# Kernel tuning notes

Measured on AMD Instinct MI355X. Metric: run time of the kernel, lower is better.

Reference implementation:

```python
import jax, jax.numpy as jnp
import numpy as np

# ----- config (mirrors SpatialAxis init) -----
B, N = 1, 32768
D_MODEL, NHEAD, DEPTH = 256, 8, 2
COORD = 3
PATCH = 512          # self.patch_size default
BITS = 10            # self.morton_bits default
SHIFT = True         # self.shift_order default
MLP_H = 4 * D_MODEL
HD = D_MODEL // NHEAD
EPS = 1e-5


def _part1by2(v):
    # spread low 10 bits of int32 so there are 2 zero bits between each
    v = v & 0x000003FF
    v = (v | (v << 16)) & 0x030000FF
    v = (v | (v << 8)) & 0x0300F00F
    v = (v | (v << 4)) & 0x030C30C3
    v = (v | (v << 2)) & 0x09249249
    return v


def _perm_for_block(coords, i):
    # Z-order (Morton) serialization with per-block axis rotation; odd blocks
    # shift the order by half a patch (shifted-window style). Returns [B,N] int32.
    c = jax.lax.stop_gradient(coords)[..., np.roll(np.arange(COORD), -i)]
    cmin = c.min(axis=1, keepdims=True)
    cmax = c.max(axis=1, keepdims=True)
    q = ((c - cmin) / (cmax - cmin + 1e-9) * (2 ** BITS - 1)).astype(jnp.int32)
    q = jnp.clip(q, 0, 2 ** BITS - 1)
    code = (_part1by2(q[..., 0]) | (_part1by2(q[..., 1]) << 1)
            | (_part1by2(q[..., 2]) << 2))  # [B,N]
    perm = jnp.argsort(code, axis=1)
    if SHIFT and (i % 2 == 1):
        perm = jnp.roll(perm, PATCH // 2, axis=1)
    return perm


def _ln(x, g, b):
    m = x.mean(-1, keepdims=True)
    v = x.var(-1, keepdims=True)
    return (x - m) * jax.lax.rsqrt(v + EPS) * g + b


def _point_block(xs, cs, p):
    # xs: [M, P, D] tokens of one patch each; cs: [M, P, 3]
    M, P, D = xs.shape
    h = _ln(xs, p['ln1_g'], p['ln1_b'])
    qkv = h @ p['w_qkv'] + p['b_qkv']                         # [M,P,3D]
    q, k, v = jnp.split(qkv, 3, axis=-1)
    q = q.reshape(M, P, NHEAD, HD)
    k = k.reshape(M, P, NHEAD, HD)
    v = v.reshape(M, P, NHEAD, HD)
    scores = jnp.einsum('mphd,mqhd->mhpq', q, k) / np.sqrt(HD).astype(np.float32)
    rel = cs[:, :, None, :] - cs[:, None, :, :]               # [M,P,P,3]
    bias = jnp.einsum('mpqc,ch->mhpq', rel, p['w_pos']) + p['b_pos'][None, :, None, None]
    attn = jax.nn.softmax(scores + bias, axis=-1)
    o = jnp.einsum('mhpq,mqhd->mphd', attn, v).reshape(M, P, D)
    xs = xs + o @ p['w_proj'] + p['b_proj']
    h2 = _ln(xs, p['ln2_g'], p['ln2_b'])
    xs = xs + jax.nn.gelu(h2 @ p['w_fc1'] + p['b_fc1']) @ p['w_fc2'] + p['b_fc2']
    return xs


def _forward(x, coords, params):
    Cc = coords.shape[-1]
    nblk = N // PATCH
    for i in range(DEPTH):
        p = {k: v[i] for k, v in params.items()}
        perm = _perm_for_block(coords, i)                      # [B,N]
        inv = jnp.argsort(perm, axis=1)
        x_s = jnp.take_along_axis(x, perm[:, :, None], axis=1)
        c_s = jnp.take_along_axis(coords, perm[:, :, None], axis=1)
        x_f = x_s.reshape(B * nblk, PATCH, D_MODEL)
        c_f = c_s.reshape(B * nblk, PATCH, Cc)
        y = _point_block(x_f, c_f, p).reshape(B, N, D_MODEL)
        x = jnp.take_along_axis(y, inv[:, :, None], axis=1)
    return _ln(x, params['norm_g'][0], params['norm_b'][0])


def setup_inputs() -> dict:
    key = jax.random.key(0)
    ks = jax.random.split(key, 20)
    s = 0.02
    d = {
        'x': jax.random.normal(ks[0], (B, N, D_MODEL), jnp.float32),
        'coords': jax.random.uniform(ks[1], (B, N, COORD), jnp.float32),
        'ln1_g': jnp.ones((DEPTH, D_MODEL), jnp.float32),
        'ln1_b': jnp.zeros((DEPTH, D_MODEL), jnp.float32),
        'w_qkv': jax.random.normal(ks[2], (DEPTH, D_MODEL, 3 * D_MODEL), jnp.float32) * s,
        'b_qkv': jnp.zeros((DEPTH, 3 * D_MODEL), jnp.float32),
        'w_proj': jax.random.normal(ks[3], (DEPTH, D_MODEL, D_MODEL), jnp.float32) * s,
        'b_proj': jnp.zeros((DEPTH, D_MODEL), jnp.float32),
        'w_pos': jax.random.normal(ks[4], (DEPTH, COORD, NHEAD), jnp.float32) * s,
        'b_pos': jnp.zeros((DEPTH, NHEAD), jnp.float32),
        'ln2_g': jnp.ones((DEPTH, D_MODEL), jnp.float32),
        'ln2_b': jnp.zeros((DEPTH, D_MODEL), jnp.float32),
        'w_fc1': jax.random.normal(ks[5], (DEPTH, D_MODEL, MLP_H), jnp.float32) * s,
        'b_fc1': jnp.zeros((DEPTH, MLP_H), jnp.float32),
        'w_fc2': jax.random.normal(ks[6], (DEPTH, MLP_H, D_MODEL), jnp.float32) * s,
        'b_fc2': jnp.zeros((DEPTH, D_MODEL), jnp.float32),
        'norm_g': jnp.ones((1, D_MODEL), jnp.float32),
        'norm_b': jnp.zeros((1, D_MODEL), jnp.float32),
    }
    return d


def reference(x, coords, ln1_g, ln1_b, w_qkv, b_qkv, w_proj, b_proj, w_pos, b_pos,
              ln2_g, ln2_b, w_fc1, b_fc1, w_fc2, b_fc2, norm_g, norm_b):
    params = dict(ln1_g=ln1_g, ln1_b=ln1_b, w_qkv=w_qkv, b_qkv=b_qkv,
                  w_proj=w_proj, b_proj=b_proj, w_pos=w_pos, b_pos=b_pos,
                  ln2_g=ln2_g, ln2_b=ln2_b, w_fc1=w_fc1, b_fc1=b_fc1,
                  w_fc2=w_fc2, b_fc2=b_fc2, norm_g=norm_g, norm_b=norm_b)
    return _forward(x, coords, params)
```

## Files before the change

kernel.cpp:

```cpp
#include <hip/hip_runtime.h>

typedef unsigned long long u64;
typedef unsigned int u32;
typedef unsigned short u16;
typedef float f32x4 __attribute__((ext_vector_type(4)));
typedef __bf16 bf16x8 __attribute__((ext_vector_type(8)));

#define N_TOK 32768

__device__ inline u16 f2bf(float f){
  u32 x = __float_as_uint(f);
  u32 r = x + 0x7FFFu + ((x >> 16) & 1u);
  return (u16)(r >> 16);
}

__device__ inline f32x4 mfma16(bf16x8 a, bf16x8 b, f32x4 c){
  return __builtin_amdgcn_mfma_f32_16x16x32_bf16(a, b, c, 0, 0, 0);
}

typedef const __attribute__((address_space(1))) unsigned int* gas_ptr;
typedef __attribute__((address_space(3))) unsigned int* las_ptr;
__device__ inline void gload_lds16(const u16* g, u16* l){
  __builtin_amdgcn_global_load_lds((gas_ptr)g, (las_ptr)l, 16, 0, 0);
}

__device__ inline u32 rp_idx(const u64* __restrict__ keys, int j, int shift){
  return (u32)(keys[(j + N_TOK - shift) & (N_TOK - 1)] & 0xFFFFull);
}

__device__ inline float gelu_tanh(float x){
  float u = 0.7978845608028654f * (x + 0.044715f * x * x * x);
  float e = __expf(2.0f * u);
  return 0.5f * x * (2.0f - 2.0f / (e + 1.0f));
}

__device__ inline u32 part1by2(u32 v){
  v &= 0x3FFu;
  v = (v | (v << 16)) & 0x030000FFu;
  v = (v | (v << 8))  & 0x0300F00Fu;
  v = (v | (v << 4))  & 0x030C30C3u;
  v = (v | (v << 2))  & 0x09249249u;
  return v;
}

__device__ inline void ce64(u64& a, u64& b, bool asc){
  u64 lo = a < b ? a : b;
  u64 hi = a < b ? b : a;
  a = asc ? lo : hi;
  b = asc ? hi : lo;
}

__global__ void __launch_bounds__(1024) minmax_kernel(const float* __restrict__ coords,
                                                      float* __restrict__ cmm){
  float mn[3] = {1e30f,1e30f,1e30f}, mx[3] = {-1e30f,-1e30f,-1e30f};
  for (int t = threadIdx.x; t < N_TOK; t += 1024){
    #pragma unroll
    for (int a = 0; a < 3; ++a){
      float v = coords[t*3 + a];
      mn[a] = fminf(mn[a], v); mx[a] = fmaxf(mx[a], v);
    }
  }
  #pragma unroll
  for (int a = 0; a < 3; ++a){
    for (int m = 1; m < 64; m <<= 1){
      mn[a] = fminf(mn[a], __shfl_xor(mn[a], m));
      mx[a] = fmaxf(mx[a], __shfl_xor(mx[a], m));
    }
  }
  __shared__ float smn[16][3], smx[16][3];
  int w = threadIdx.x >> 6, lane = threadIdx.x & 63;
  if (lane == 0){
    #pragma unroll
    for (int a = 0; a < 3; ++a){ smn[w][a] = mn[a]; smx[w][a] = mx[a]; }
  }
  __syncthreads();
  if (threadIdx.x == 0){
    for (int i = 1; i < 16; ++i)
      for (int a = 0; a < 3; ++a){
        smn[0][a] = fminf(smn[0][a], smn[i][a]);
        smx[0][a] = fmaxf(smx[0][a], smx[i][a]);
      }
    for (int a = 0; a < 3; ++a){ cmm[a] = smn[0][a]; cmm[3+a] = smx[0][a]; }
  }
}

__global__ void __launch_bounds__(256) wprep_kernel(const float* __restrict__ src,
                                                    u16* __restrict__ dst, int K, int Nn){
  int layer = blockIdx.y;
  src += (size_t)layer * K * Nn;
  dst += (size_t)layer * K * Nn;
  int ntx = Nn >> 5;
  int tk = blockIdx.x / ntx, tn = blockIdx.x % ntx;
  __shared__ float tile[32][33];
  int r = threadIdx.x >> 5, c = threadIdx.x & 31;
  for (int rr = r; rr < 32; rr += 8)
    tile[rr][c] = src[(size_t)(tk*32 + rr) * Nn + tn*32 + c];
  __syncthreads();
  for (int rr = r; rr < 32; rr += 8)
    dst[(size_t)(tn*32 + rr) * K + tk*32 + c] = f2bf(tile[c][rr]);
}

__global__ void __launch_bounds__(256) codes_kernel(const float* __restrict__ coords,
                                                    const float* __restrict__ cmm,
                                                    u64* __restrict__ keys){
  int p = blockIdx.x * 256 + threadIdx.x;
  int layer = p >> 15, t = p & (N_TOK - 1);
  u32 code = 0;
  #pragma unroll
  for (int j = 0; j < 3; ++j){
    int ax = (j + layer) % 3;
    float c = coords[t*3 + ax];
    float mn = cmm[ax], mx = cmm[3 + ax];
    float v = (c - mn) / (mx - mn + 1e-9f) * 1023.0f;
    int q = (int)v;
    q = q < 0 ? 0 : (q > 1023 ? 1023 : q);
    code |= part1by2((u32)q) << j;
  }
  keys[p] = ((u64)code << 16) | (u32)t;
}

__global__ void __launch_bounds__(512) bitonic_local_sort8k(u64* __restrict__ keys){
  __shared__ u64 s[8192];
  int base = blockIdx.x * 8192;
  int tid = threadIdx.x;
  {
    int c = tid * 16;
    u64 v[16];
    #pragma unroll
    for (int p = 0; p < 16; ++p) v[p] = keys[base + c + p];
    #pragma unroll
    for (int k2 = 2; k2 <= 16; k2 <<= 1){
      #pragma unroll
      for (int j = k2 >> 1; j > 0; j >>= 1){
        #pragma unroll
        for (int p = 0; p < 16; ++p){
          if ((p & j) == 0){
            bool asc = ((((base + c + p) & (N_TOK-1)) & k2) == 0);
            ce64(v[p], v[p+j], asc);
          }
        }
      }
    }
    #pragma unroll
    for (int p = 0; p < 16; ++p) s[c + p] = v[p];
  }
  __syncthreads();
  for (int k = 32; k <= 8192; k <<= 1){
    int j = k >> 1;
    while (j >= 16){
      if (j >= 32){
        int j2 = j >> 1;
        int bb[4]; bool aa[4]; u64 e[4][4];
        #pragma unroll
        for (int it = 0; it < 4; ++it){
          int g = tid + it*512;
          int lo = g & (j2 - 1);
          int b = ((g ^ lo) << 2) | lo;
          bb[it] = b;
          aa[it] = ((((base + b) & (N_TOK-1)) & k) == 0);
          e[it][0] = s[b]; e[it][1] = s[b + j2]; e[it][2] = s[b + j]; e[it][3] = s[b + j + j2];
        }
        #pragma unroll
        for (int it = 0; it < 4; ++it){
          ce64(e[it][0], e[it][2], aa[it]); ce64(e[it][1], e[it][3], aa[it]);
          ce64(e[it][0], e[it][1], aa[it]); ce64(e[it][2], e[it][3], aa[it]);
          s[bb[it]] = e[it][0]; s[bb[it]+j2] = e[it][1];
          s[bb[it]+j] = e[it][2]; s[bb[it]+j+j2] = e[it][3];
        }
        j >>= 2;
      } else {
        int ii[8]; bool aa[8]; u64 ea[8], eb[8];
        #pragma unroll
        for (int it = 0; it < 8; ++it){
          int pr = tid + it*512;
          int i = ((pr & ~15) << 1) | (pr & 15);
          ii[it] = i;
          aa[it] = ((((base + i) & (N_TOK-1)) & k) == 0);
          ea[it] = s[i]; eb[it] = s[i + 16];
        }
        #pragma unroll
        for (int it = 0; it < 8; ++it){
          ce64(ea[it], eb[it], aa[it]);
          s[ii[it]] = ea[it]; s[ii[it]+16] = eb[it];
        }
        j >>= 1;
      }
      __syncthreads();
    }
    {
      int c = tid * 16;
      bool asc = ((((base + c) & (N_TOK-1)) & k) == 0);
      u64 v[16];
      #pragma unroll
      for (int p = 0; p < 16; ++p) v[p] = s[c + p];
      #pragma unroll
      for (int j2 = 8; j2 > 0; j2 >>= 1){
        #pragma unroll
        for (int p = 0; p < 16; ++p)
          if ((p & j2) == 0) ce64(v[p], v[p+j2], asc);
      }
      if (k == 8192){
        #pragma unroll
        for (int p = 0; p < 16; ++p) keys[base + c + p] = v[p];
      } else {
        #pragma unroll
        for (int p = 0; p < 16; ++p) s[c + p] = v[p];
        __syncthreads();
      }
    }
  }
}

__global__ void __launch_bounds__(256) bitonic_global_step(u64* __restrict__ keys, int j, int k){
  int p = blockIdx.x * 256 + threadIdx.x;
  int layer = p >> 14, pl = p & 16383;
  int i = ((pl & ~(j-1)) << 1) | (pl & (j-1));
  int l = i + j;
  bool asc = ((i & k & (N_TOK-1)) == 0);
  u64* kp = keys + (layer << 15);
  u64 a = kp[i], b = kp[l];
  if ((a > b) == asc){ kp[i] = b; kp[l] = a; }
}

__global__ void __launch_bounds__(512) bitonic_local_merge8k(u64* __restrict__ keys, int k){
  __shared__ u64 s[8192];
  int base = blockIdx.x * 8192;
  int tid = threadIdx.x;
  for (int i = tid; i < 8192; i += 512) s[i] = keys[base + i];
  __syncthreads();
  int j = 4096;
  while (j >= 16){
    if (j >= 32){
      int j2 = j >> 1;
      int bb[4]; bool aa[4]; u64 e[4][4];
      #pragma unroll
      for (int it = 0; it < 4; ++it){
        int g = tid + it*512;
        int lo = g & (j2 - 1);
        int b = ((g ^ lo) << 2) | lo;
        bb[it] = b;
        aa[it] = ((((base + b) & (N_TOK-1)) & k) == 0);
        e[it][0] = s[b]; e[it][1] = s[b + j2]; e[it][2] = s[b + j]; e[it][3] = s[b + j + j2];
      }
      #pragma unroll
      for (int it = 0; it < 4; ++it){
        ce64(e[it][0], e[it][2], aa[it]); ce64(e[it][1], e[it][3], aa[it]);
        ce64(e[it][0], e[it][1], aa[it]); ce64(e[it][2], e[it][3], aa[it]);
        s[bb[it]] = e[it][0]; s[bb[it]+j2] = e[it][1];
        s[bb[it]+j] = e[it][2]; s[bb[it]+j+j2] = e[it][3];
      }
      j >>= 2;
    } else {
      int ii[8]; bool aa[8]; u64 ea[8], eb[8];
      #pragma unroll
      for (int it = 0; it < 8; ++it){
        int pr = tid + it*512;
        int i = ((pr & ~15) << 1) | (pr & 15);
        ii[it] = i;
        aa[it] = ((((base + i) & (N_TOK-1)) & k) == 0);
        ea[it] = s[i]; eb[it] = s[i + 16];
      }
      #pragma unroll
      for (int it = 0; it < 8; ++it){
        ce64(ea[it], eb[it], aa[it]);
        s[ii[it]] = ea[it]; s[ii[it]+16] = eb[it];
      }
      j >>= 1;
    }
    __syncthreads();
  }
  int c = tid * 16;
  bool asc = ((((base + c) & (N_TOK-1)) & k) == 0);
  u64 v[16];
  #pragma unroll
  for (int p = 0; p < 16; ++p) v[p] = s[c + p];
  #pragma unroll
  for (int j2 = 8; j2 > 0; j2 >>= 1){
    #pragma unroll
    for (int p = 0; p < 16; ++p)
      if ((p & j2) == 0) ce64(v[p], v[p+j2], asc);
  }
  #pragma unroll
  for (int p = 0; p < 16; ++p) keys[base + c + p] = v[p];
}

__global__ void __launch_bounds__(256) gather_ln1_kernel(
    const float* __restrict__ xin, const float* __restrict__ coords,
    const u64* __restrict__ keys, int shift,
    const float* __restrict__ g1, const float* __restrict__ b1,
    const float* __restrict__ wpos,
    float* __restrict__ dproj, u16* __restrict__ h){
  int w = threadIdx.x >> 6, lane = threadIdx.x & 63;
  int j = blockIdx.x * 4 + w;
  u32 src = rp_idx(keys, j, shift);
  float4 v = ((const float4*)xin)[(size_t)src * 64 + lane];
  float s = v.x + v.y + v.z + v.w;
  for (int m = 1; m < 64; m <<= 1) s += __shfl_xor(s, m);
  float mean = s * (1.0f / 256.0f);
  float dx = v.x - mean, dy = v.y - mean, dz = v.z - mean, dw = v.w - mean;
  float q = dx*dx + dy*dy + dz*dz + dw*dw;
  for (int m = 1; m < 64; m <<= 1) q += __shfl_xor(q, m);
  float rs = rsqrtf(q * (1.0f / 256.0f) + 1e-5f);
  int c0 = lane * 4;
  u16 h0 = f2bf(dx * rs * g1[c0+0] + b1[c0+0]);
  u16 h1 = f2bf(dy * rs * g1[c0+1] + b1[c0+1]);
  u16 h2 = f2bf(dz * rs * g1[c0+2] + b1[c0+2]);
  u16 h3 = f2bf(dw * rs * g1[c0+3] + b1[c0+3]);
  uint2 pk; pk.x = (u32)h0 | ((u32)h1 << 16); pk.y = (u32)h2 | ((u32)h3 << 16);
  *(uint2*)&h[(size_t)j * 256 + c0] = pk;
  if (lane < 8){
    float acc = 0.0f;
    #pragma unroll
    for (int c = 0; c < 3; ++c) acc += coords[(size_t)src*3 + c] * wpos[c*8 + lane];
    dproj[(size_t)j * 8 + lane] = acc;
  }
}

__global__ void __launch_bounds__(256) ln_bf16_kernel(const float* __restrict__ xin,
    const float* __restrict__ g, const float* __restrict__ b, u16* __restrict__ out){
  int w = threadIdx.x >> 6, lane = threadIdx.x & 63;
  int j = blockIdx.x * 4 + w;
  float4 v = ((const float4*)xin)[(size_t)j * 64 + lane];
  float s = v.x + v.y + v.z + v.w;
  for (int m = 1; m < 64; m <<= 1) s += __shfl_xor(s, m);
  float mean = s * (1.0f / 256.0f);
  float dx = v.x - mean, dy = v.y - mean, dz = v.z - mean, dw = v.w - mean;
  float q = dx*dx + dy*dy + dz*dz + dw*dw;
  for (int m = 1; m < 64; m <<= 1) q += __shfl_xor(q, m);
  float rs = rsqrtf(q * (1.0f / 256.0f) + 1e-5f);
  int c0 = lane * 4;
  u16 h0 = f2bf(dx * rs * g[c0+0] + b[c0+0]);
  u16 h1 = f2bf(dy * rs * g[c0+1] + b[c0+1]);
  u16 h2 = f2bf(dz * rs * g[c0+2] + b[c0+2]);
  u16 h3 = f2bf(dw * rs * g[c0+3] + b[c0+3]);
  uint2 pk; pk.x = (u32)h0 | ((u32)h1 << 16); pk.y = (u32)h2 | ((u32)h3 << 16);
  *(uint2*)&out[(size_t)j * 256 + c0] = pk;
}

__global__ void __launch_bounds__(256) ln_final_kernel(const float* __restrict__ xin,
    const float* __restrict__ g, const float* __restrict__ b, float* __restrict__ out){
  int w = threadIdx.x >> 6, lane = threadIdx.x & 63;
  int j = blockIdx.x * 4 + w;
  float4 v = ((const float4*)xin)[(size_t)j * 64 + lane];
  float s = v.x + v.y + v.z + v.w;
  for (int m = 1; m < 64; m <<= 1) s += __shfl_xor(s, m);
  float mean = s * (1.0f / 256.0f);
  float dx = v.x - mean, dy = v.y - mean, dz = v.z - mean, dw = v.w - mean;
  float q = dx*dx + dy*dy + dz*dz + dw*dw;
  for (int m = 1; m < 64; m <<= 1) q += __shfl_xor(q, m);
  float rs = rsqrtf(q * (1.0f / 256.0f) + 1e-5f);
  int c0 = lane * 4;
  float4 o;
  o.x = dx * rs * g[c0+0] + b[c0+0];
  o.y = dy * rs * g[c0+1] + b[c0+1];
  o.z = dz * rs * g[c0+2] + b[c0+2];
  o.w = dw * rs * g[c0+3] + b[c0+3];
  ((float4*)out)[(size_t)j * 64 + lane] = o;
}

template<int EPI>
__global__ void __launch_bounds__(256) gemm_kernel(
    const u16* __restrict__ A, const u16* __restrict__ Wt,
    const float* __restrict__ bias, int K, int Nn,
    u16* __restrict__ outb, float* __restrict__ outf,
    const float* __restrict__ res, const u64* __restrict__ keys, int shift){
  __shared__ __align__(16) u16 As[2][128 * 32];
  __shared__ __align__(16) u16 Bs[2][128 * 32];
  int m0 = blockIdx.x * 128;
  int n0 = blockIdx.y * 128;
  int tid = threadIdx.x;
  int lane = tid & 63, lc = lane & 15, g = lane >> 4;
  int w = tid >> 6, wm = w >> 1, wn = w & 1;
  f32x4 acc[4][4];
  #pragma unroll
  for (int mi = 0; mi < 4; ++mi)
    #pragma unroll
    for (int ni = 0; ni < 4; ++ni) acc[mi][ni] = (f32x4){0.f,0.f,0.f,0.f};
  int r1 = tid >> 2, s1 = tid & 3;
  int r2 = r1 + 64;
  const u16* Ag1 = A  + (size_t)(m0 + r1) * K + s1*8;
  const u16* Ag2 = A  + (size_t)(m0 + r2) * K + s1*8;
  const u16* Bg1 = Wt + (size_t)(n0 + r1) * K + s1*8;
  const u16* Bg2 = Wt + (size_t)(n0 + r2) * K + s1*8;
  int wofs = (tid & ~63) * 8;
  int nt = K >> 5;
  gload_lds16(Ag1, As[0] + wofs);
  gload_lds16(Ag2, As[0] + wofs + 2048);
  gload_lds16(Bg1, Bs[0] + wofs);
  gload_lds16(Bg2, Bs[0] + wofs + 2048);
  __syncthreads();
  int cur = 0;
  for (int t = 0; t < nt; ++t){
    if (t + 1 < nt){
      int kk = (t + 1) << 5;
      gload_lds16(Ag1 + kk, As[cur^1] + wofs);
      gload_lds16(Ag2 + kk, As[cur^1] + wofs + 2048);
      gload_lds16(Bg1 + kk, Bs[cur^1] + wofs);
      gload_lds16(Bg2 + kk, Bs[cur^1] + wofs + 2048);
    }
    bf16x8 af[4], bfr[4];
    #pragma unroll
    for (int mi = 0; mi < 4; ++mi)
      af[mi] = *(const bf16x8*)&As[cur][(wm*64 + mi*16 + lc)*32 + g*8];
    #pragma unroll
    for (int ni = 0; ni < 4; ++ni)
      bfr[ni] = *(const bf16x8*)&Bs[cur][(wn*64 + ni*16 + lc)*32 + g*8];
    #pragma unroll
    for (int mi = 0; mi < 4; ++mi)
      #pragma unroll
      for (int ni = 0; ni < 4; ++ni)
        acc[mi][ni] = mfma16(af[mi], bfr[ni], acc[mi][ni]);
    __syncthreads();
    cur ^= 1;
  }
  #pragma unroll
  for (int ni = 0; ni < 4; ++ni){
    int col = n0 + wn*64 + ni*16 + lc;
    float bv = bias[col];
    #pragma unroll
    for (int mi = 0; mi < 4; ++mi){
      #pragma unroll
      for (int r = 0; r < 4; ++r){
        int row = m0 + wm*64 + mi*16 + g*4 + r;
        float v = acc[mi][ni][r] + bv;
        if constexpr (EPI == 0){
          if (col < 256) v *= 0.25500526f;
          outb[(size_t)row * Nn + col] = f2bf(v);
        } else if constexpr (EPI == 1){
          outb[(size_t)row * Nn + col] = f2bf(gelu_tanh(v));
        } else if constexpr (EPI == 2){
          u32 src = rp_idx(keys, row, shift);
          outf[(size_t)row * 256 + col] = res[(size_t)src * 256 + col] + v;
        } else {
          u32 dst = rp_idx(keys, row, shift);
          outf[(size_t)dst * 256 + col] = res[(size_t)row * 256 + col] + v;
        }
      }
    }
  }
}

#define VSTR 516
#define ATTN_LDS (512*40*2 + 32*VSTR*2 + 512*2)
__global__ void __launch_bounds__(512) attn_kernel(
    const u16* __restrict__ qkvb, const float* __restrict__ dproj,
    u16* __restrict__ o){
  extern __shared__ char smem[];
  u16* Kl = (u16*)smem;
  u16* Vt = (u16*)(smem + 512*40*2);
  u16* wl = (u16*)(smem + 512*40*2 + 32*VSTR*2);
  int h = blockIdx.x & 7;
  int base = (blockIdx.x >> 3) * 512;
  int tid = threadIdx.x, w = tid >> 6, lane = tid & 63, lc = lane & 15, g = lane >> 4;
  const float L2E = 1.4426950408889634f;
  for (int i = tid; i < 2048; i += 512){
    int j = i >> 2, s = i & 3;
    *(uint4*)&Kl[j*40 + s*8] =
      *(const uint4*)&qkvb[(size_t)(base + j)*768 + 256 + h*32 + s*8];
  }
  for (int i = tid; i < 1024; i += 512){
    int p = i >> 2, d0 = (i & 3) * 8;
    int j0 = 2*p, j1 = j0 + 1;
    float wv0 = exp2f(-L2E * dproj[(size_t)(base + j0)*8 + h]);
    float wv1 = exp2f(-L2E * dproj[(size_t)(base + j1)*8 + h]);
    uint4 r0 = *(const uint4*)&qkvb[(size_t)(base + j0)*768 + 512 + h*32 + d0];
    uint4 r1 = *(const uint4*)&qkvb[(size_t)(base + j1)*768 + 512 + h*32 + d0];
    const u16* p0 = (const u16*)&r0; const u16* p1 = (const u16*)&r1;
    int j5 = j0 & 31, b = j5 >> 4, m = j5 & 15;
    int slot = (j0 & ~31) + 8*(m >> 2) + 4*b + (m & 3);
    #pragma unroll
    for (int e = 0; e < 8; ++e){
      float f0 = __uint_as_float(((u32)p0[e]) << 16) * wv0;
      float f1 = __uint_as_float(((u32)p1[e]) << 16) * wv1;
      u32 pk;
      asm("v_cvt_pk_bf16_f32 %0, %1, %2" : "=v"(pk) : "v"(f0), "v"(f1));
      *(u32*)&Vt[(d0 + e)*VSTR + slot] = pk;
    }
    if (d0 == 0){
      u32 pkw;
      asm("v_cvt_pk_bf16_f32 %0, %1, %2" : "=v"(pkw) : "v"(wv0), "v"(wv1));
      *(u32*)&wl[slot] = pkw;
    }
  }
  __syncthreads();
  const f32x4 zf = {0.f,0.f,0.f,0.f};
  const bf16x8 zb = {};
  const u16* Qg = qkvb + (size_t)base*768 + h*32;
  for (int t = 0; t < 4; ++t){
    int q0 = w*64 + t*16;
    bf16x8 qf = *(const bf16x8*)&Qg[(size_t)(q0 + lc)*768 + g*8];
    f32x4 o0 = zf, o1 = zf, lacc = zf;
    #pragma unroll 4
    for (int grp = 0; grp < 16; ++grp){
      int kb = grp * 32;
      bf16x8 kf0 = *(const bf16x8*)&Kl[(kb + lc)*40 + g*8];
      bf16x8 kf1 = *(const bf16x8*)&Kl[(kb + 16 + lc)*40 + g*8];
      f32x4 s0 = mfma16(kf0, qf, zf);
      f32x4 s1 = mfma16(kf1, qf, zf);
      #pragma unroll
      for (int r = 0; r < 4; ++r){
        s0[r] = exp2f(s0[r]);
        s1[r] = exp2f(s1[r]);
      }
      u32 pk0, pk1, pk2, pk3;
      asm("v_cvt_pk_bf16_f32 %0, %1, %2" : "=v"(pk0) : "v"(s0[0]), "v"(s0[1]));
      asm("v_cvt_pk_bf16_f32 %0, %1, %2" : "=v"(pk1) : "v"(s0[2]), "v"(s0[3]));
      asm("v_cvt_pk_bf16_f32 %0, %1, %2" : "=v"(pk2) : "v"(s1[0]), "v"(s1[1]));
      asm("v_cvt_pk_bf16_f32 %0, %1, %2" : "=v"(pk3) : "v"(s1[2]), "v"(s1[3]));
      bf16x8 pf;
      ((u32*)&pf)[0] = pk0; ((u32*)&pf)[1] = pk1;
      ((u32*)&pf)[2] = pk2; ((u32*)&pf)[3] = pk3;
      bf16x8 v0, v1;
      *(uint2*)&v0       = *(const uint2*)&Vt[lc*VSTR + kb + g*8];
      *((uint2*)&v0 + 1) = *(const uint2*)&Vt[lc*VSTR + kb + g*8 + 4];
      *(uint2*)&v1       = *(const uint2*)&Vt[(16+lc)*VSTR + kb + g*8];
      *((uint2*)&v1 + 1) = *(const uint2*)&Vt[(16+lc)*VSTR + kb + g*8 + 4];
      bf16x8 wf = *(const bf16x8*)&wl[kb + g*8];
      bf16x8 wfz = (lc == 0) ? wf : zb;
      __builtin_amdgcn_s_setprio(1);
      o0 = mfma16(pf, v0, o0);
      o1 = mfma16(pf, v1, o1);
      lacc = mfma16(pf, wfz, lacc);
      __builtin_amdgcn_s_setprio(0);
    }
    #pragma unroll
    for (int r = 0; r < 4; ++r){
      float l = __shfl(lacc[r], lane & 48);
      float inv = 1.0f / l;
      size_t tok = (size_t)(base + q0 + g*4 + r);
      o[tok*256 + h*32 + lc]      = f2bf(o0[r] * inv);
      o[tok*256 + h*32 + 16 + lc] = f2bf(o1[r] * inv);
    }
  }
}

extern "C" void kernel_launch(void* const* d_in, const int* in_sizes, int n_in,
                              void* d_out, int out_size, void* d_ws, size_t ws_size,
                              hipStream_t stream){
  const float* x      = (const float*)d_in[0];
  const float* coords = (const float*)d_in[1];
  const float* ln1_g  = (const float*)d_in[2];
  const float* ln1_b  = (const float*)d_in[3];
  const float* w_qkv  = (const float*)d_in[4];
  const float* b_qkv  = (const float*)d_in[5];
  const float* w_proj = (const float*)d_in[6];
  const float* b_proj = (const float*)d_in[7];
  const float* w_pos  = (const float*)d_in[8];
  const float* ln2_g  = (const float*)d_in[10];
  const float* ln2_b  = (const float*)d_in[11];
  const float* w_fc1  = (const float*)d_in[12];
  const float* b_fc1  = (const float*)d_in[13];
  const float* w_fc2  = (const float*)d_in[14];
  const float* b_fc2  = (const float*)d_in[15];
  const float* norm_g = (const float*)d_in[16];
  const float* norm_b = (const float*)d_in[17];
  float* outp = (float*)d_out;

  hipFuncSetAttribute((const void*)attn_kernel,
                      hipFuncAttributeMaxDynamicSharedMemorySize, ATTN_LDS);

  char* ws = (char*)d_ws;
  size_t off = 0;
  auto alloc = [&](size_t bytes) -> void* {
    void* p = ws + off;
    off += (bytes + 255) & ~(size_t)255;
    return p;
  };
  u64*   keys   = (u64*)  alloc((size_t)2 * N_TOK * 8);
  float* cmm    = (float*)alloc(256);
  float* dproj  = (float*)alloc((size_t)N_TOK * 8 * 4);
  u16*   h      = (u16*)  alloc((size_t)N_TOK * 256 * 2);
  u16*   qkvb   = (u16*)  alloc((size_t)N_TOK * 768 * 2);
  float* x2     = (float*)alloc((size_t)N_TOK * 256 * 4);
  u16*   t      = (u16*)  alloc((size_t)N_TOK * 1024 * 2);
  float* xA     = (float*)alloc((size_t)N_TOK * 256 * 4);
  u16*   wtqkv  = (u16*)  alloc((size_t)2 * 256 * 768 * 2);
  u16*   wtproj = (u16*)  alloc((size_t)2 * 256 * 256 * 2);
  u16*   wtfc1  = (u16*)  alloc((size_t)2 * 256 * 1024 * 2);
  u16*   wtfc2  = (u16*)  alloc((size_t)2 * 1024 * 256 * 2);
  u16*   o      = t;
  float* xB     = (float*)qkvb;
  (void)in_sizes; (void)n_in; (void)out_size; (void)ws_size;

  minmax_kernel<<<1, 1024, 0, stream>>>(coords, cmm);
  wprep_kernel<<<dim3(8*24, 2),  256, 0, stream>>>(w_qkv,  wtqkv,  256, 768);
  wprep_kernel<<<dim3(8*8, 2),   256, 0, stream>>>(w_proj, wtproj, 256, 256);
  wprep_kernel<<<dim3(8*32, 2),  256, 0, stream>>>(w_fc1,  wtfc1,  256, 1024);
  wprep_kernel<<<dim3(32*8, 2),  256, 0, stream>>>(w_fc2,  wtfc2,  1024, 256);

  codes_kernel<<<256, 256, 0, stream>>>(coords, cmm, keys);
  bitonic_local_sort8k<<<8, 512, 0, stream>>>(keys);
  bitonic_global_step<<<128, 256, 0, stream>>>(keys, 8192, 16384);
  bitonic_local_merge8k<<<8, 512, 0, stream>>>(keys, 16384);
  bitonic_global_step<<<128, 256, 0, stream>>>(keys, 16384, 32768);
  bitonic_global_step<<<128, 256, 0, stream>>>(keys, 8192, 32768);
  bitonic_local_merge8k<<<8, 512, 0, stream>>>(keys, 32768);

  for (int layer = 0; layer < 2; ++layer){
    int shift = (layer & 1) ? 256 : 0;
    const float* xin = (layer == 0) ? x : xA;
    float* xout = (layer == 0) ? xA : xB;
    u64* keyL = keys + (size_t)layer * N_TOK;

    gather_ln1_kernel<<<8192, 256, 0, stream>>>(xin, coords, keyL, shift,
        ln1_g + layer*256, ln1_b + layer*256, w_pos + layer*24, dproj, h);
    gemm_kernel<0><<<dim3(256, 6), 256, 0, stream>>>(h, wtqkv + (size_t)layer*768*256,
        b_qkv + layer*768, 256, 768, qkvb, nullptr, nullptr, nullptr, 0);
    attn_kernel<<<512, 512, ATTN_LDS, stream>>>(qkvb, dproj, o);
    gemm_kernel<2><<<dim3(256, 2), 256, 0, stream>>>(o, wtproj + (size_t)layer*256*256,
        b_proj + layer*256, 256, 256, nullptr, x2, xin, keyL, shift);
    ln_bf16_kernel<<<8192, 256, 0, stream>>>(x2, ln2_g + layer*256, ln2_b + layer*256, h);
    gemm_kernel<1><<<dim3(256, 8), 256, 0, stream>>>(h, wtfc1 + (size_t)layer*1024*256,
        b_fc1 + layer*1024, 256, 1024, t, nullptr, nullptr, nullptr, 0);
    gemm_kernel<3><<<dim3(256, 2), 256, 0, stream>>>(t, wtfc2 + (size_t)layer*256*1024,
        b_fc2 + layer*256, 1024, 256, nullptr, xout, x2, keyL, shift);
  }
  ln_final_kernel<<<8192, 256, 0, stream>>>(xB, norm_g, norm_b, outp);
}
```

Before: 561.2 us.

## Replace LDS bitonic sort with wave-shuffle and strided multi-step global passes

The single-block min/max reduction becomes a grid-wide reduction: shared-memory atomics on float bit patterns, then global atomics. The bitonic sort drops its 8-block LDS kernels for wave-level kernels that sort and merge 1024-key chunks with register shuffles, plus strided kernels that do several compare-exchange levels per global pass. The aim is more parallelism than the 8-block sort allows, at the cost of more kernel launches and more global memory traffic. The unsigned-compare min/max trick is only correct for non-negative coordinates.

Result: faster. 547.9 us (-2.4%).

```diff
diff --git a/kernel.cpp b/kernel.cpp
--- a/kernel.cpp
+++ b/kernel.cpp
@@ -50,37 +50,27 @@
   b = asc ? hi : lo;
 }
 
-__global__ void __launch_bounds__(1024) minmax_kernel(const float* __restrict__ coords,
-                                                      float* __restrict__ cmm){
-  float mn[3] = {1e30f,1e30f,1e30f}, mx[3] = {-1e30f,-1e30f,-1e30f};
-  for (int t = threadIdx.x; t < N_TOK; t += 1024){
-    #pragma unroll
-    for (int a = 0; a < 3; ++a){
-      float v = coords[t*3 + a];
-      mn[a] = fminf(mn[a], v); mx[a] = fmaxf(mx[a], v);
-    }
-  }
-  #pragma unroll
-  for (int a = 0; a < 3; ++a){
-    for (int m = 1; m < 64; m <<= 1){
-      mn[a] = fminf(mn[a], __shfl_xor(mn[a], m));
-      mx[a] = fmaxf(mx[a], __shfl_xor(mx[a], m));
-    }
-  }
-  __shared__ float smn[16][3], smx[16][3];
-  int w = threadIdx.x >> 6, lane = threadIdx.x & 63;
-  if (lane == 0){
-    #pragma unroll
-    for (int a = 0; a < 3; ++a){ smn[w][a] = mn[a]; smx[w][a] = mx[a]; }
-  }
+__global__ void minmax_init(u32* __restrict__ cmm){
+  int t = threadIdx.x;
+  if (t < 3) cmm[t] = 0xFFFFFFFFu;
+  else if (t < 6) cmm[t] = 0u;
+}
+
+__global__ void __launch_bounds__(256) minmax_atomic(const float* __restrict__ coords,
+                                                     u32* __restrict__ cmm){
+  __shared__ u32 smn[3], smx[3];
+  int t = threadIdx.x;
+  if (t < 3){ smn[t] = 0xFFFFFFFFu; smx[t] = 0u; }
   __syncthreads();
-  if (threadIdx.x == 0){
-    for (int i = 1; i < 16; ++i)
-      for (int a = 0; a < 3; ++a){
-        smn[0][a] = fminf(smn[0][a], smn[i][a]);
-        smx[0][a] = fmaxf(smx[0][a], smx[i][a]);
-      }
-    for (int a = 0; a < 3; ++a){ cmm[a] = smn[0][a]; cmm[3+a] = smx[0][a]; }
+  int i = blockIdx.x * 256 + t;
+  u32 bits = __float_as_uint(coords[i]);
+  int a = i % 3;
+  atomicMin(&smn[a], bits);
+  atomicMax(&smx[a], bits);
+  __syncthreads();
+  if (t < 3){
+    atomicMin(&cmm[t], smn[t]);
+    atomicMax(&cmm[3 + t], smx[t]);
   }
 }
 
@@ -119,169 +109,99 @@
   keys[p] = ((u64)code << 16) | (u32)t;
 }
 
-__global__ void __launch_bounds__(512) bitonic_local_sort8k(u64* __restrict__ keys){
-  __shared__ u64 s[8192];
-  int base = blockIdx.x * 8192;
-  int tid = threadIdx.x;
-  {
-    int c = tid * 16;
-    u64 v[16];
-    #pragma unroll
-    for (int p = 0; p < 16; ++p) v[p] = keys[base + c + p];
-    #pragma unroll
-    for (int k2 = 2; k2 <= 16; k2 <<= 1){
+__global__ void __launch_bounds__(64) sort_wave1024(u64* __restrict__ keys){
+  int chunk = blockIdx.x;
+  int lane = threadIdx.x;
+  int base = chunk * 1024 + lane * 16;
+  int bl = base & (N_TOK - 1);
+  u64 v[16];
+  #pragma unroll
+  for (int p = 0; p < 16; ++p) v[p] = keys[base + p];
+  #pragma unroll
+  for (int k2 = 2; k2 <= 16; k2 <<= 1){
+    #pragma unroll
+    for (int j = k2 >> 1; j > 0; j >>= 1){
       #pragma unroll
-      for (int j = k2 >> 1; j > 0; j >>= 1){
-        #pragma unroll
-        for (int p = 0; p < 16; ++p){
-          if ((p & j) == 0){
-            bool asc = ((((base + c + p) & (N_TOK-1)) & k2) == 0);
-            ce64(v[p], v[p+j], asc);
-          }
+      for (int p = 0; p < 16; ++p){
+        if ((p & j) == 0){
+          bool asc = (((bl + p) & k2) == 0);
+          ce64(v[p], v[p+j], asc);
         }
       }
     }
-    #pragma unroll
-    for (int p = 0; p < 16; ++p) s[c + p] = v[p];
-  }
-  __syncthreads();
-  for (int k = 32; k <= 8192; k <<= 1){
-    int j = k >> 1;
-    while (j >= 16){
-      if (j >= 32){
-        int j2 = j >> 1;
-        int bb[4]; bool aa[4]; u64 e[4][4];
-        #pragma unroll
-        for (int it = 0; it < 4; ++it){
-          int g = tid + it*512;
-          int lo = g & (j2 - 1);
-          int b = ((g ^ lo) << 2) | lo;
-          bb[it] = b;
-          aa[it] = ((((base + b) & (N_TOK-1)) & k) == 0);
-          e[it][0] = s[b]; e[it][1] = s[b + j2]; e[it][2] = s[b + j]; e[it][3] = s[b + j + j2];
-        }
-        #pragma unroll
-        for (int it = 0; it < 4; ++it){
-          ce64(e[it][0], e[it][2], aa[it]); ce64(e[it][1], e[it][3], aa[it]);
-          ce64(e[it][0], e[it][1], aa[it]); ce64(e[it][2], e[it][3], aa[it]);
-          s[bb[it]] = e[it][0]; s[bb[it]+j2] = e[it][1];
-          s[bb[it]+j] = e[it][2]; s[bb[it]+j+j2] = e[it][3];
-        }
-        j >>= 2;
-      } else {
-        int ii[8]; bool aa[8]; u64 ea[8], eb[8];
-        #pragma unroll
-        for (int it = 0; it < 8; ++it){
-          int pr = tid + it*512;
-          int i = ((pr & ~15) << 1) | (pr & 15);
-          ii[it] = i;
-          aa[it] = ((((base + i) & (N_TOK-1)) & k) == 0);
-          ea[it] = s[i]; eb[it] = s[i + 16];
-        }
-        #pragma unroll
-        for (int it = 0; it < 8; ++it){
-          ce64(ea[it], eb[it], aa[it]);
-          s[ii[it]] = ea[it]; s[ii[it]+16] = eb[it];
-        }
-        j >>= 1;
+  }
+  #pragma unroll
+  for (int kk = 32; kk <= 1024; kk <<= 1){
+    bool asc = ((bl & kk) == 0);
+    #pragma unroll
+    for (int j = kk >> 1; j >= 16; j >>= 1){
+      int m = j >> 4;
+      bool kmin = asc != ((lane & m) != 0);
+      #pragma unroll
+      for (int p = 0; p < 16; ++p){
+        u64 pv = __shfl_xor(v[p], m);
+        u64 mn = v[p] < pv ? v[p] : pv;
+        u64 mx = v[p] < pv ? pv : v[p];
+        v[p] = kmin ? mn : mx;
       }
-      __syncthreads();
-    }
-    {
-      int c = tid * 16;
-      bool asc = ((((base + c) & (N_TOK-1)) & k) == 0);
-      u64 v[16];
+    }
+    #pragma unroll
+    for (int j = 8; j > 0; j >>= 1)
       #pragma unroll
-      for (int p = 0; p < 16; ++p) v[p] = s[c + p];
-      #pragma unroll
-      for (int j2 = 8; j2 > 0; j2 >>= 1){
-        #pragma unroll
-        for (int p = 0; p < 16; ++p)
-          if ((p & j2) == 0) ce64(v[p], v[p+j2], asc);
-      }
-      if (k == 8192){
-        #pragma unroll
-        for (int p = 0; p < 16; ++p) keys[base + c + p] = v[p];
-      } else {
-        #pragma unroll
-        for (int p = 0; p < 16; ++p) s[c + p] = v[p];
-        __syncthreads();
-      }
-    }
-  }
-}
-
-__global__ void __launch_bounds__(256) bitonic_global_step(u64* __restrict__ keys, int j, int k){
-  int p = blockIdx.x * 256 + threadIdx.x;
-  int layer = p >> 14, pl = p & 16383;
-  int i = ((pl & ~(j-1)) << 1) | (pl & (j-1));
-  int l = i + j;
-  bool asc = ((i & k & (N_TOK-1)) == 0);
-  u64* kp = keys + (layer << 15);
-  u64 a = kp[i], b = kp[l];
-  if ((a > b) == asc){ kp[i] = b; kp[l] = a; }
-}
-
-__global__ void __launch_bounds__(512) bitonic_local_merge8k(u64* __restrict__ keys, int k){
-  __shared__ u64 s[8192];
-  int base = blockIdx.x * 8192;
-  int tid = threadIdx.x;
-  for (int i = tid; i < 8192; i += 512) s[i] = keys[base + i];
-  __syncthreads();
-  int j = 4096;
-  while (j >= 16){
-    if (j >= 32){
-      int j2 = j >> 1;
-      int bb[4]; bool aa[4]; u64 e[4][4];
-      #pragma unroll
-      for (int it = 0; it < 4; ++it){
-        int g = tid + it*512;
-        int lo = g & (j2 - 1);
-        int b = ((g ^ lo) << 2) | lo;
-        bb[it] = b;
-        aa[it] = ((((base + b) & (N_TOK-1)) & k) == 0);
-        e[it][0] = s[b]; e[it][1] = s[b + j2]; e[it][2] = s[b + j]; e[it][3] = s[b + j + j2];
-      }
-      #pragma unroll
-      for (int it = 0; it < 4; ++it){
-        ce64(e[it][0], e[it][2], aa[it]); ce64(e[it][1], e[it][3], aa[it]);
-        ce64(e[it][0], e[it][1], aa[it]); ce64(e[it][2], e[it][3], aa[it]);
-        s[bb[it]] = e[it][0]; s[bb[it]+j2] = e[it][1];
-        s[bb[it]+j] = e[it][2]; s[bb[it]+j+j2] = e[it][3];
-      }
-      j >>= 2;
-    } else {
-      int ii[8]; bool aa[8]; u64 ea[8], eb[8];
-      #pragma unroll
-      for (int it = 0; it < 8; ++it){
-        int pr = tid + it*512;
-        int i = ((pr & ~15) << 1) | (pr & 15);
-        ii[it] = i;
-        aa[it] = ((((base + i) & (N_TOK-1)) & k) == 0);
-        ea[it] = s[i]; eb[it] = s[i + 16];
-      }
-      #pragma unroll
-      for (int it = 0; it < 8; ++it){
-        ce64(ea[it], eb[it], aa[it]);
-        s[ii[it]] = ea[it]; s[ii[it]+16] = eb[it];
-      }
-      j >>= 1;
-    }
-    __syncthreads();
-  }
-  int c = tid * 16;
-  bool asc = ((((base + c) & (N_TOK-1)) & k) == 0);
+      for (int p = 0; p < 16; ++p)
+        if ((p & j) == 0) ce64(v[p], v[p+j], asc);
+  }
+  #pragma unroll
+  for (int p = 0; p < 16; ++p) keys[base + p] = v[p];
+}
+
+template<int R>
+__global__ void __launch_bounds__(256) sort_strided(u64* __restrict__ keys, int logJ, int k){
+  const int E = 1 << R;
+  int gps = N_TOK >> R;
+  int tid = blockIdx.x * 256 + threadIdx.x;
+  int seg = tid / gps, gamma = tid % gps;
+  int high = gamma >> logJ, low = gamma & ((1 << logJ) - 1);
+  int base = seg * N_TOK + (high << (logJ + R)) + low;
+  u64 v[E];
+  #pragma unroll
+  for (int m = 0; m < E; ++m) v[m] = keys[base + (m << logJ)];
+  bool asc = (((base & (N_TOK - 1)) & k) == 0);
+  #pragma unroll
+  for (int jj = R - 1; jj >= 0; --jj)
+    #pragma unroll
+    for (int m = 0; m < E; ++m)
+      if ((m & (1 << jj)) == 0) ce64(v[m], v[m + (1 << jj)], asc);
+  #pragma unroll
+  for (int m = 0; m < E; ++m) keys[base + (m << logJ)] = v[m];
+}
+
+__global__ void __launch_bounds__(64) sort_tail1024(u64* __restrict__ keys, int k){
+  int chunk = blockIdx.x;
+  int lane = threadIdx.x;
+  int base = chunk * 1024 + lane * 16;
+  bool asc = ((((chunk * 1024) & (N_TOK - 1)) & k) == 0);
   u64 v[16];
   #pragma unroll
-  for (int p = 0; p < 16; ++p) v[p] = s[c + p];
-  #pragma unroll
-  for (int j2 = 8; j2 > 0; j2 >>= 1){
+  for (int p = 0; p < 16; ++p) v[p] = keys[base + p];
+  #pragma unroll
+  for (int m = 32; m >= 1; m >>= 1){
+    bool kmin = asc != ((lane & m) != 0);
+    #pragma unroll
+    for (int p = 0; p < 16; ++p){
+      u64 pv = __shfl_xor(v[p], m);
+      u64 mn = v[p] < pv ? v[p] : pv;
+      u64 mx = v[p] < pv ? pv : v[p];
+      v[p] = kmin ? mn : mx;
+    }
+  }
+  #pragma unroll
+  for (int j = 8; j > 0; j >>= 1)
     #pragma unroll
     for (int p = 0; p < 16; ++p)
-      if ((p & j2) == 0) ce64(v[p], v[p+j2], asc);
-  }
-  #pragma unroll
-  for (int p = 0; p < 16; ++p) keys[base + c + p] = v[p];
+      if ((p & j) == 0) ce64(v[p], v[p+j], asc);
+  #pragma unroll
+  for (int p = 0; p < 16; ++p) keys[base + p] = v[p];
 }
 
 __global__ void __launch_bounds__(256) gather_ln1_kernel(
@@ -582,19 +502,27 @@
   float* xB     = (float*)qkvb;
   (void)in_sizes; (void)n_in; (void)out_size; (void)ws_size;
 
-  minmax_kernel<<<1, 1024, 0, stream>>>(coords, cmm);
+  minmax_init<<<1, 64, 0, stream>>>((u32*)cmm);
+  minmax_atomic<<<384, 256, 0, stream>>>(coords, (u32*)cmm);
   wprep_kernel<<<dim3(8*24, 2),  256, 0, stream>>>(w_qkv,  wtqkv,  256, 768);
   wprep_kernel<<<dim3(8*8, 2),   256, 0, stream>>>(w_proj, wtproj, 256, 256);
   wprep_kernel<<<dim3(8*32, 2),  256, 0, stream>>>(w_fc1,  wtfc1,  256, 1024);
   wprep_kernel<<<dim3(32*8, 2),  256, 0, stream>>>(w_fc2,  wtfc2,  1024, 256);
 
   codes_kernel<<<256, 256, 0, stream>>>(coords, cmm, keys);
-  bitonic_local_sort8k<<<8, 512, 0, stream>>>(keys);
-  bitonic_global_step<<<128, 256, 0, stream>>>(keys, 8192, 16384);
-  bitonic_local_merge8k<<<8, 512, 0, stream>>>(keys, 16384);
-  bitonic_global_step<<<128, 256, 0, stream>>>(keys, 16384, 32768);
-  bitonic_global_step<<<128, 256, 0, stream>>>(keys, 8192, 32768);
-  bitonic_local_merge8k<<<8, 512, 0, stream>>>(keys, 32768);
+  sort_wave1024<<<64, 64, 0, stream>>>(keys);
+  sort_strided<1><<<128, 256, 0, stream>>>(keys, 10, 2048);
+  sort_tail1024<<<64, 64, 0, stream>>>(keys, 2048);
+  sort_strided<2><<<64, 256, 0, stream>>>(keys, 10, 4096);
+  sort_tail1024<<<64, 64, 0, stream>>>(keys, 4096);
+  sort_strided<3><<<32, 256, 0, stream>>>(keys, 10, 8192);
+  sort_tail1024<<<64, 64, 0, stream>>>(keys, 8192);
+  sort_strided<3><<<32, 256, 0, stream>>>(keys, 11, 16384);
+  sort_strided<1><<<128, 256, 0, stream>>>(keys, 10, 16384);
+  sort_tail1024<<<64, 64, 0, stream>>>(keys, 16384);
+  sort_strided<3><<<32, 256, 0, stream>>>(keys, 12, 32768);
+  sort_strided<2><<<64, 256, 0, stream>>>(keys, 10, 32768);
+  sort_tail1024<<<64, 64, 0, stream>>>(keys, 32768);
 
   for (int layer = 0; layer < 2; ++layer){
     int shift = (layer & 1) ? 256 : 0;
```
